# Performance work log

Measured on AMD Instinct MI355X. Metric: run time of the kernel, lower is better.

Reference implementation:

```python
import jax, jax.numpy as jnp
import numpy as np

N_NODES = 100000
FEAT = 64
HID = 128
N_EDGES = 1200000


def setup_inputs() -> dict:
    key = jax.random.key(0)
    ks = jax.random.split(key, 8)
    x = jax.random.normal(ks[0], (N_NODES, FEAT), dtype=jnp.float32)
    edge_index = jax.random.randint(ks[1], (2, N_EDGES), 0, N_NODES, dtype=jnp.int32)
    # SAGEConv params: lin_l (on aggregated neighbors, with bias), lin_r (on root, no bias)
    W1l = jax.random.normal(ks[2], (HID, FEAT), jnp.float32) / np.float32(np.sqrt(FEAT))
    b1l = jnp.zeros((HID,), jnp.float32)
    W1r = jax.random.normal(ks[3], (HID, FEAT), jnp.float32) / np.float32(np.sqrt(FEAT))
    W2l = jax.random.normal(ks[4], (FEAT, HID), jnp.float32) / np.float32(np.sqrt(HID))
    b2l = jnp.zeros((FEAT,), jnp.float32)
    W2r = jax.random.normal(ks[5], (FEAT, HID), jnp.float32) / np.float32(np.sqrt(HID))
    return {"x": x, "edge_index": edge_index, "W1l": W1l, "b1l": b1l,
            "W1r": W1r, "W2l": W2l, "b2l": b2l, "W2r": W2r}


def _sage_conv(x, src, dst, Wl, bl, Wr, n_nodes):
    # mean aggregation of neighbor messages x[src] at targets dst
    msg = x[src]                                                  # [E, d]
    agg = jax.ops.segment_sum(msg, dst, num_segments=n_nodes)     # [N, d]
    deg = jax.ops.segment_sum(jnp.ones((src.shape[0],), x.dtype), dst,
                              num_segments=n_nodes)               # [N]
    agg = agg / jnp.maximum(deg, 1.0)[:, None]
    # out = lin_l(agg) + lin_r(x); lin_r has no bias (PyG SAGEConv default)
    return agg @ Wl.T + bl + x @ Wr.T


def reference(x, edge_index, W1l, b1l, W1r, W2l, b2l, W2r):
    src, dst = edge_index[0], edge_index[1]
    n = x.shape[0]
    h = jax.nn.relu(_sage_conv(x, src, dst, W1l, b1l, W1r, n))
    # dropout(p=0.5) is identity in eval mode
    out = _sage_conv(h, src, dst, W2l, b2l, W2r, n)
    return out
```

## Files before the change

### kernel.cpp

```cpp
#include <hip/hip_runtime.h>
#include <hip/hip_bf16.h>

typedef __bf16 bf16;
typedef __attribute__((ext_vector_type(8))) __bf16 bf16x8;
typedef __attribute__((ext_vector_type(4))) float f32x4;

#define NBLK 256

__device__ inline void unpack8(uint4 r, f32x4& a, f32x4& b) {
  a.x = __uint_as_float(r.x << 16);
  a.y = __uint_as_float(r.x & 0xffff0000u);
  a.z = __uint_as_float(r.y << 16);
  a.w = __uint_as_float(r.y & 0xffff0000u);
  b.x = __uint_as_float(r.z << 16);
  b.y = __uint_as_float(r.z & 0xffff0000u);
  b.z = __uint_as_float(r.w << 16);
  b.w = __uint_as_float(r.w & 0xffff0000u);
}

__device__ inline uint4 slot_load(const bf16* __restrict__ tab, const int* __restrict__ nbr,
                                  int base, int e, int q, int fo) {
  int idx = base + q;
  uint4 r = make_uint4(0u, 0u, 0u, 0u);
  if (idx < e) {
    int j = nbr[idx];
    r = *(const uint4*)(tab + j * 64 + fo);
  }
  return r;
}

__global__ __launch_bounds__(256) void setup_k(const float* __restrict__ x,
                                               const int* __restrict__ dst,
                                               const float* __restrict__ W1l,
                                               const float* __restrict__ W1r,
                                               const float* __restrict__ W2l,
                                               const float* __restrict__ W2r,
                                               bf16* __restrict__ xb,
                                               bf16* __restrict__ B1,
                                               bf16* __restrict__ B2,
                                               int* __restrict__ hist,
                                               int E, int nb, int N, int Np) {
  __shared__ int h[1024];
  int t = threadIdx.x;
  if (blockIdx.x < NBLK) {
    for (int i = t; i < nb; i += 256) h[i] = 0;
    __syncthreads();
    int chunk = (E + NBLK - 1) / NBLK;
    int s = blockIdx.x * chunk, e = min(E, s + chunk);
    for (int i = s + t; i < e; i += 256) atomicAdd(&h[dst[i] >> 7], 1);
    __syncthreads();
    for (int i = t; i < nb; i += 256) hist[(long)i * NBLK + blockIdx.x] = h[i];
  } else if (blockIdx.x < NBLK + 128) {
    int gid = (blockIdx.x - NBLK) * 256 + t;
    if (gid < 16384) {
      int c = gid >> 7, k = gid & 127;
      float v = (k < 64) ? W1l[c * 64 + k] : W1r[c * 64 + (k - 64)];
      B1[gid] = (bf16)v;
    } else {
      int idx = gid - 16384;
      int n = idx >> 7, k = idx & 127;
      float v = (n < 64) ? W2l[n * 128 + k] : W2r[(n - 64) * 128 + k];
      B2[idx] = (bf16)v;
    }
  } else {
    int gid = (blockIdx.x - NBLK - 128) * 256 + t;
    long base = (long)gid * 4;
    if (base >= (long)Np * 64) return;
    if (base < (long)N * 64) {
      f32x4 v = *(const f32x4*)(x + base);
      bf16 o[4] = {(bf16)v.x, (bf16)v.y, (bf16)v.z, (bf16)v.w};
      *(ulong1*)(xb + base) = *(ulong1*)o;
    } else {
      bf16 o[4] = {(bf16)0.0f, (bf16)0.0f, (bf16)0.0f, (bf16)0.0f};
      *(ulong1*)(xb + base) = *(ulong1*)o;
    }
  }
}

__global__ __launch_bounds__(256) void scanA_k(int* __restrict__ hist,
                                               int* __restrict__ bsum) {
  __shared__ int sd[256];
  int t = threadIdx.x;
  int idx = blockIdx.x * 256 + t;
  int v = hist[idx];
  sd[t] = v;
  __syncthreads();
#pragma unroll
  for (int off = 1; off < 256; off <<= 1) {
    int tv = (t >= off) ? sd[t - off] : 0;
    __syncthreads();
    if (t >= off) sd[t] += tv;
    __syncthreads();
  }
  hist[idx] = sd[t] - v;
  if (t == 255) bsum[blockIdx.x] = sd[255];
}

__global__ __launch_bounds__(1024) void scanB_k(int* __restrict__ bsum, int nb) {
  __shared__ int sd[1024];
  int t = threadIdx.x;
  int v = (t < nb) ? bsum[t] : 0;
  sd[t] = v;
  __syncthreads();
#pragma unroll
  for (int off = 1; off < 1024; off <<= 1) {
    int tv = (t >= off) ? sd[t - off] : 0;
    __syncthreads();
    if (t >= off) sd[t] += tv;
    __syncthreads();
  }
  if (t < nb) bsum[t] = sd[t] - v;
}

__global__ __launch_bounds__(512) void scat_k(const int* __restrict__ src,
                                              const int* __restrict__ dst,
                                              const int* __restrict__ hist,
                                              const int* __restrict__ bsum,
                                              unsigned* __restrict__ ebuf, int E, int nb) {
  __shared__ int cur[1024];
  for (int i = threadIdx.x; i < nb; i += 512)
    cur[i] = bsum[i] + hist[(long)i * NBLK + blockIdx.x];
  __syncthreads();
  int chunk = (E + NBLK - 1) / NBLK;
  int s = blockIdx.x * chunk, e = min(E, s + chunk);
  for (int i = s + threadIdx.x; i < e; i += 512) {
    int d = dst[i];
    int pos = atomicAdd(&cur[d >> 7], 1);
    ebuf[pos] = ((unsigned)src[i] << 7) | (unsigned)(d & 127);
  }
}

__global__ __launch_bounds__(256) void csr_k(const unsigned* __restrict__ ebuf,
                                             const int* __restrict__ bsum,
                                             int* __restrict__ rowptr,
                                             int* __restrict__ nbr, int nb, int Np, int E) {
  __shared__ int hcnt[128];
  __shared__ int hoff[128];
  int b = blockIdx.x, t = threadIdx.x;
  int s = bsum[b];
  int e = (b + 1 < nb) ? bsum[b + 1] : E;
  if (t < 128) hcnt[t] = 0;
  __syncthreads();
  for (int i = s + t; i < e; i += 256) atomicAdd(&hcnt[ebuf[i] & 127u], 1);
  __syncthreads();
  if (t < 128) hoff[t] = hcnt[t];
  __syncthreads();
#pragma unroll
  for (int off = 1; off < 128; off <<= 1) {
    int v = (t < 128 && t >= off) ? hoff[t - off] : 0;
    __syncthreads();
    if (t < 128 && t >= off) hoff[t] += v;
    __syncthreads();
  }
  if (t < 128) {
    int ex = hoff[t] - hcnt[t];
    rowptr[b * 128 + t] = s + ex;
    hcnt[t] = ex;
  }
  if (blockIdx.x == gridDim.x - 1 && t == 0) rowptr[Np] = E;
  __syncthreads();
  for (int i = s + t; i < e; i += 256) {
    unsigned r = ebuf[i];
    int pos = atomicAdd(&hcnt[r & 127u], 1);
    nbr[s + pos] = (int)(r >> 7);
  }
}

__global__ __launch_bounds__(256) void agg1_k(const bf16* __restrict__ xb,
                                              const int* __restrict__ rowptr,
                                              const int* __restrict__ nbr,
                                              bf16* __restrict__ A1, int Np) {
  int wave = threadIdx.x >> 6, lane = threadIdx.x & 63;
  int n = blockIdx.x * 4 + wave;
  if (n >= Np) return;
  int s = rowptr[n], e = rowptr[n + 1];
  int q = lane >> 3, f = lane & 7;
  int fo = f * 8;
  f32x4 sa = {0, 0, 0, 0}, sb = {0, 0, 0, 0};
  uint4 c0 = slot_load(xb, nbr, s, e, q, fo);
  uint4 c1 = slot_load(xb, nbr, s + 8, e, q, fo);
  int i = s + 16;
  for (; i < e; i += 16) {
    uint4 n0 = slot_load(xb, nbr, i, e, q, fo);
    uint4 n1 = slot_load(xb, nbr, i + 8, e, q, fo);
    f32x4 a, b;
    unpack8(c0, a, b); sa += a; sb += b;
    unpack8(c1, a, b); sa += a; sb += b;
    c0 = n0; c1 = n1;
  }
  {
    f32x4 a, b;
    unpack8(c0, a, b); sa += a; sb += b;
    unpack8(c1, a, b); sa += a; sb += b;
  }
  float v[8] = {sa.x, sa.y, sa.z, sa.w, sb.x, sb.y, sb.z, sb.w};
#pragma unroll
  for (int k = 0; k < 8; k++) {
    v[k] += __shfl_xor(v[k], 8);
    v[k] += __shfl_xor(v[k], 16);
    v[k] += __shfl_xor(v[k], 32);
  }
  float invd = 1.0f / fmaxf((float)(e - s), 1.0f);
  if (q == 0) {
    bf16x8 o = {(bf16)(v[0] * invd), (bf16)(v[1] * invd), (bf16)(v[2] * invd),
                (bf16)(v[3] * invd), (bf16)(v[4] * invd), (bf16)(v[5] * invd),
                (bf16)(v[6] * invd), (bf16)(v[7] * invd)};
    *(bf16x8*)(A1 + n * 128 + fo) = o;
  } else if (q == 1) {
    uint4 rv = *(const uint4*)(xb + n * 64 + fo);
    *(uint4*)(A1 + n * 128 + 64 + fo) = rv;
  }
}

__device__ inline int swzoff(int r, int x) {
  return r * 256 + (x ^ (((r & 3) << 6) ^ ((r & 7) << 4)));
}

__global__ __launch_bounds__(256) void fused_k(const bf16* __restrict__ A,
                                               const bf16* __restrict__ B1g,
                                               const bf16* __restrict__ B2g,
                                               const float* __restrict__ b1l,
                                               bf16* __restrict__ Ct,
                                               bf16* __restrict__ Cu, int T) {
  __shared__ __align__(16) char Asm[2][8192];
  __shared__ __align__(16) char Hsm[8192];
  int tid = threadIdx.x;
  int wave = tid >> 6, lane = tid & 63;
  int row = lane & 15, quad = lane >> 4;
  int cb = wave * 32;

  bf16x8 b1f[2][4], b2f[2][4];
#pragma unroll
  for (int jj = 0; jj < 2; jj++)
#pragma unroll
    for (int s = 0; s < 4; s++) {
      b1f[jj][s] = *(const bf16x8*)(B1g + (cb + jj * 16 + row) * 128 + s * 32 + quad * 8);
      b2f[jj][s] = *(const bf16x8*)(B2g + (cb + jj * 16 + row) * 128 + s * 32 + quad * 8);
    }
  float bias[2] = {b1l[cb + row], b1l[cb + 16 + row]};

  int srow = wave * 8 + quad;
  int schunk = row;

  int t = blockIdx.x;
  {
    uint4 v0 = *(const uint4*)(A + ((long)t * 32 + srow) * 128 + schunk * 8);
    uint4 v1 = *(const uint4*)(A + ((long)t * 32 + srow + 4) * 128 + schunk * 8);
    *(uint4*)(Asm[0] + swzoff(srow, schunk * 16)) = v0;
    *(uint4*)(Asm[0] + swzoff(srow + 4, schunk * 16)) = v1;
  }
  __syncthreads();

  int p = 0;
  for (; t < T; t += (int)gridDim.x, p ^= 1) {
    int tn = t + (int)gridDim.x;
    bool pf = tn < T;
    uint4 v0 = {}, v1 = {};
    if (pf) {
      v0 = *(const uint4*)(A + ((long)tn * 32 + srow) * 128 + schunk * 8);
      v1 = *(const uint4*)(A + ((long)tn * 32 + srow + 4) * 128 + schunk * 8);
    }
    f32x4 acc1[2][2] = {};
#pragma unroll
    for (int s = 0; s < 4; s++) {
#pragma unroll
      for (int st = 0; st < 2; st++) {
        bf16x8 a = *(const bf16x8*)(Asm[p] + swzoff(st * 16 + row, s * 64 + quad * 16));
#pragma unroll
        for (int jj = 0; jj < 2; jj++)
          acc1[st][jj] = __builtin_amdgcn_mfma_f32_16x16x32_bf16(a, b1f[jj][s], acc1[st][jj], 0, 0, 0);
      }
    }
#pragma unroll
    for (int st = 0; st < 2; st++)
#pragma unroll
      for (int jj = 0; jj < 2; jj++)
#pragma unroll
        for (int i = 0; i < 4; i++) {
          float v = acc1[st][jj][i] + bias[jj];
          v = v > 0.0f ? v : 0.0f;
          *(bf16*)(Hsm + swzoff(st * 16 + quad * 4 + i, (cb + jj * 16 + row) * 2)) = (bf16)v;
        }
    __syncthreads();
    f32x4 acc2[2][2] = {};
#pragma unroll
    for (int s = 0; s < 4; s++) {
#pragma unroll
      for (int st = 0; st < 2; st++) {
        bf16x8 a = *(const bf16x8*)(Hsm + swzoff(st * 16 + row, s * 64 + quad * 16));
#pragma unroll
        for (int jj = 0; jj < 2; jj++)
          acc2[st][jj] = __builtin_amdgcn_mfma_f32_16x16x32_bf16(a, b2f[jj][s], acc2[st][jj], 0, 0, 0);
      }
    }
    bf16* outp = (wave < 2) ? Ct : Cu;
    int oc = cb + row - ((wave < 2) ? 0 : 64);
#pragma unroll
    for (int st = 0; st < 2; st++)
#pragma unroll
      for (int jj = 0; jj < 2; jj++)
#pragma unroll
        for (int i = 0; i < 4; i++) {
          long grow = (long)t * 32 + st * 16 + quad * 4 + i;
          outp[grow * 64 + oc + jj * 16] = (bf16)acc2[st][jj][i];
        }
    if (pf) {
      *(uint4*)(Asm[p ^ 1] + swzoff(srow, schunk * 16)) = v0;
      *(uint4*)(Asm[p ^ 1] + swzoff(srow + 4, schunk * 16)) = v1;
    }
    __syncthreads();
  }
}

__global__ __launch_bounds__(256) void agg2_k(const bf16* __restrict__ tmat,
                                              const bf16* __restrict__ umat,
                                              const int* __restrict__ rowptr,
                                              const int* __restrict__ nbr,
                                              const float* __restrict__ b2l,
                                              float* __restrict__ out, int N) {
  int wave = threadIdx.x >> 6, lane = threadIdx.x & 63;
  int n = blockIdx.x * 4 + wave;
  if (n >= N) return;
  int s = rowptr[n], e = rowptr[n + 1];
  int q = lane >> 3, f = lane & 7;
  int fo = f * 8;
  f32x4 sa = {0, 0, 0, 0}, sb = {0, 0, 0, 0};
  uint4 c0 = slot_load(tmat, nbr, s, e, q, fo);
  uint4 c1 = slot_load(tmat, nbr, s + 8, e, q, fo);
  int i = s + 16;
  for (; i < e; i += 16) {
    uint4 n0 = slot_load(tmat, nbr, i, e, q, fo);
    uint4 n1 = slot_load(tmat, nbr, i + 8, e, q, fo);
    f32x4 a, b;
    unpack8(c0, a, b); sa += a; sb += b;
    unpack8(c1, a, b); sa += a; sb += b;
    c0 = n0; c1 = n1;
  }
  {
    f32x4 a, b;
    unpack8(c0, a, b); sa += a; sb += b;
    unpack8(c1, a, b); sa += a; sb += b;
  }
  float v[8] = {sa.x, sa.y, sa.z, sa.w, sb.x, sb.y, sb.z, sb.w};
#pragma unroll
  for (int k = 0; k < 8; k++) {
    v[k] += __shfl_xor(v[k], 8);
    v[k] += __shfl_xor(v[k], 16);
    v[k] += __shfl_xor(v[k], 32);
  }
  if (q == 0) {
    float invd = 1.0f / fmaxf((float)(e - s), 1.0f);
    f32x4 b0 = *(const f32x4*)(b2l + fo);
    f32x4 b1 = *(const f32x4*)(b2l + fo + 4);
    f32x4 ua, ub;
    unpack8(*(const uint4*)(umat + n * 64 + fo), ua, ub);
    f32x4 o0, o1;
    o0.x = v[0] * invd + b0.x + ua.x;
    o0.y = v[1] * invd + b0.y + ua.y;
    o0.z = v[2] * invd + b0.z + ua.z;
    o0.w = v[3] * invd + b0.w + ua.w;
    o1.x = v[4] * invd + b1.x + ub.x;
    o1.y = v[5] * invd + b1.y + ub.y;
    o1.z = v[6] * invd + b1.z + ub.z;
    o1.w = v[7] * invd + b1.w + ub.w;
    *(f32x4*)(out + n * 64 + fo) = o0;
    *(f32x4*)(out + n * 64 + fo + 4) = o1;
  }
}

static inline size_t align256(size_t x) { return (x + 255) / 256 * 256; }

extern "C" void kernel_launch(void* const* d_in, const int* in_sizes, int n_in,
                              void* d_out, int out_size, void* d_ws, size_t ws_size,
                              hipStream_t stream) {
  const float* x = (const float*)d_in[0];
  const int* edge_index = (const int*)d_in[1];
  const float* W1l = (const float*)d_in[2];
  const float* b1l = (const float*)d_in[3];
  const float* W1r = (const float*)d_in[4];
  const float* W2l = (const float*)d_in[5];
  const float* b2l = (const float*)d_in[6];
  const float* W2r = (const float*)d_in[7];

  const int N = in_sizes[0] / 64;
  const int E = in_sizes[1] / 2;
  const int Np = (N + 127) / 128 * 128;
  const int nb = Np / 128;
  const int M = nb * NBLK;

  const int* src = edge_index;
  const int* dst = edge_index + E;

  char* ws = (char*)d_ws;
  size_t off = 0;
  int* hist = (int*)(ws + off);           off += align256((size_t)M * 4);
  int* bsum = (int*)(ws + off);           off += align256((size_t)nb * 4);
  int* rowptr = (int*)(ws + off);         off += align256((size_t)(Np + 1) * 4);
  unsigned* ebuf = (unsigned*)(ws + off); off += align256((size_t)E * 4);
  int* nbr = (int*)(ws + off);            off += align256((size_t)E * 4);
  bf16* xb = (bf16*)(ws + off);           off += align256((size_t)Np * 64 * 2);
  bf16* A1 = (bf16*)(ws + off);           off += align256((size_t)Np * 128 * 2);
  bf16* tmat = (bf16*)(ws + off);         off += align256((size_t)Np * 64 * 2);
  bf16* umat = (bf16*)(ws + off);         off += align256((size_t)Np * 64 * 2);
  bf16* B1 = (bf16*)(ws + off);           off += align256(128 * 128 * 2);
  bf16* B2 = (bf16*)(ws + off);           off += align256(128 * 128 * 2);
  float* out = (float*)d_out;

  const int cvtBlocks = (int)(((long)Np * 64 / 4 + 255) / 256);
  setup_k<<<NBLK + 128 + cvtBlocks, 256, 0, stream>>>(x, dst, W1l, W1r, W2l, W2r,
                                                      xb, B1, B2, hist, E, nb, N, Np);
  scanA_k<<<nb, 256, 0, stream>>>(hist, bsum);
  scanB_k<<<1, 1024, 0, stream>>>(bsum, nb);
  scat_k<<<NBLK, 512, 0, stream>>>(src, dst, hist, bsum, ebuf, E, nb);
  csr_k<<<nb, 256, 0, stream>>>(ebuf, bsum, rowptr, nbr, nb, Np, E);

  agg1_k<<<Np / 4, 256, 0, stream>>>(xb, rowptr, nbr, A1, Np);
  fused_k<<<1024, 256, 0, stream>>>(A1, B1, B2, b1l, tmat, umat, Np / 32);
  agg2_k<<<(N + 3) / 4, 256, 0, stream>>>(tmat, umat, rowptr, nbr, b2l, out, N);
}
```

Measured before the change: 219.2 us.

## Process four nodes per wave in agg1 with cross-node software prefetch

Result: no change. 220.2 us (+0.4%).

```diff
diff --git a/kernel.cpp b/kernel.cpp
--- a/kernel.cpp
+++ b/kernel.cpp
@@ -171,44 +171,64 @@
                                               const int* __restrict__ nbr,
                                               bf16* __restrict__ A1, int Np) {
   int wave = threadIdx.x >> 6, lane = threadIdx.x & 63;
-  int n = blockIdx.x * 4 + wave;
-  if (n >= Np) return;
-  int s = rowptr[n], e = rowptr[n + 1];
+  int n0 = (blockIdx.x * 4 + wave) * 4;
+  if (n0 >= Np) return;
   int q = lane >> 3, f = lane & 7;
   int fo = f * 8;
-  f32x4 sa = {0, 0, 0, 0}, sb = {0, 0, 0, 0};
-  uint4 c0 = slot_load(xb, nbr, s, e, q, fo);
-  uint4 c1 = slot_load(xb, nbr, s + 8, e, q, fo);
-  int i = s + 16;
-  for (; i < e; i += 16) {
-    uint4 n0 = slot_load(xb, nbr, i, e, q, fo);
-    uint4 n1 = slot_load(xb, nbr, i + 8, e, q, fo);
-    f32x4 a, b;
-    unpack8(c0, a, b); sa += a; sb += b;
-    unpack8(c1, a, b); sa += a; sb += b;
-    c0 = n0; c1 = n1;
-  }
-  {
-    f32x4 a, b;
-    unpack8(c0, a, b); sa += a; sb += b;
-    unpack8(c1, a, b); sa += a; sb += b;
-  }
-  float v[8] = {sa.x, sa.y, sa.z, sa.w, sb.x, sb.y, sb.z, sb.w};
-#pragma unroll
-  for (int k = 0; k < 8; k++) {
-    v[k] += __shfl_xor(v[k], 8);
-    v[k] += __shfl_xor(v[k], 16);
-    v[k] += __shfl_xor(v[k], 32);
-  }
-  float invd = 1.0f / fmaxf((float)(e - s), 1.0f);
-  if (q == 0) {
-    bf16x8 o = {(bf16)(v[0] * invd), (bf16)(v[1] * invd), (bf16)(v[2] * invd),
-                (bf16)(v[3] * invd), (bf16)(v[4] * invd), (bf16)(v[5] * invd),
-                (bf16)(v[6] * invd), (bf16)(v[7] * invd)};
-    *(bf16x8*)(A1 + n * 128 + fo) = o;
-  } else if (q == 1) {
-    uint4 rv = *(const uint4*)(xb + n * 64 + fo);
-    *(uint4*)(A1 + n * 128 + 64 + fo) = rv;
+  int s[4], e[4];
+#pragma unroll
+  for (int m = 0; m < 4; m++) { s[m] = rowptr[n0 + m]; e[m] = rowptr[n0 + m + 1]; }
+  uint4 c0[4], c1[4];
+#pragma unroll
+  for (int m = 0; m < 2; m++) {
+    c0[m] = slot_load(xb, nbr, s[m], e[m], q, fo);
+    c1[m] = slot_load(xb, nbr, s[m] + 8, e[m], q, fo);
+  }
+  uint4 rvc = (q == 1) ? *(const uint4*)(xb + (long)n0 * 64 + fo)
+                       : make_uint4(0u, 0u, 0u, 0u);
+#pragma unroll
+  for (int m = 0; m < 4; m++) {
+    if (m + 2 < 4) {
+      c0[m + 2] = slot_load(xb, nbr, s[m + 2], e[m + 2], q, fo);
+      c1[m + 2] = slot_load(xb, nbr, s[m + 2] + 8, e[m + 2], q, fo);
+    }
+    uint4 rvn = (q == 1 && m + 1 < 4)
+                    ? *(const uint4*)(xb + (long)(n0 + m + 1) * 64 + fo)
+                    : make_uint4(0u, 0u, 0u, 0u);
+    f32x4 sa = {0, 0, 0, 0}, sb = {0, 0, 0, 0};
+    uint4 a0 = c0[m], a1 = c1[m];
+    if (s[m] + 16 < e[m]) {
+      for (int i = s[m] + 16; i < e[m]; i += 16) {
+        uint4 t0 = slot_load(xb, nbr, i, e[m], q, fo);
+        uint4 t1 = slot_load(xb, nbr, i + 8, e[m], q, fo);
+        f32x4 a, b;
+        unpack8(a0, a, b); sa += a; sb += b;
+        unpack8(a1, a, b); sa += a; sb += b;
+        a0 = t0; a1 = t1;
+      }
+    }
+    {
+      f32x4 a, b;
+      unpack8(a0, a, b); sa += a; sb += b;
+      unpack8(a1, a, b); sa += a; sb += b;
+    }
+    float v[8] = {sa.x, sa.y, sa.z, sa.w, sb.x, sb.y, sb.z, sb.w};
+#pragma unroll
+    for (int k = 0; k < 8; k++) {
+      v[k] += __shfl_xor(v[k], 8);
+      v[k] += __shfl_xor(v[k], 16);
+      v[k] += __shfl_xor(v[k], 32);
+    }
+    float invd = 1.0f / fmaxf((float)(e[m] - s[m]), 1.0f);
+    if (q == 0) {
+      bf16x8 o = {(bf16)(v[0] * invd), (bf16)(v[1] * invd), (bf16)(v[2] * invd),
+                  (bf16)(v[3] * invd), (bf16)(v[4] * invd), (bf16)(v[5] * invd),
+                  (bf16)(v[6] * invd), (bf16)(v[7] * invd)};
+      *(bf16x8*)(A1 + (long)(n0 + m) * 128 + fo) = o;
+    } else if (q == 1) {
+      *(uint4*)(A1 + (long)(n0 + m) * 128 + 64 + fo) = rvc;
+    }
+    rvc = rvn;
   }
 }
 
@@ -414,7 +434,7 @@
   scat_k<<<NBLK, 512, 0, stream>>>(src, dst, hist, bsum, ebuf, E, nb);
   csr_k<<<nb, 256, 0, stream>>>(ebuf, bsum, rowptr, nbr, nb, Np, E);
 
-  agg1_k<<<Np / 4, 256, 0, stream>>>(xb, rowptr, nbr, A1, Np);
-  fused_k<<<1024, 256, 0, stream>>>(A1, B1, B2, b1l, tmat, umat, Np / 32);
+  agg1_k<<<Np / 16, 256, 0, stream>>>(xb, rowptr, nbr, A1, Np);
+  fused_k<<<1564, 256, 0, stream>>>(A1, B1, B2, b1l, tmat, umat, Np / 32);
   agg2_k<<<(N + 3) / 4, 256, 0, stream>>>(tmat, umat, rowptr, nbr, b2l, out, N);
 }
```

## Fuse per-bucket CSR sort into both aggregation kernels via LDS neighbor lists

Applied to the files above, without the earlier changes.

Result: slower. 228.7 us (+4.3%).

```diff
diff --git a/kernel.cpp b/kernel.cpp
--- a/kernel.cpp
+++ b/kernel.cpp
@@ -6,6 +6,7 @@
 typedef __attribute__((ext_vector_type(4))) float f32x4;
 
 #define NBLK 256
+#define CAP 3072
 
 __device__ inline void unpack8(uint4 r, f32x4& a, f32x4& b) {
   a.x = __uint_as_float(r.x << 16);
@@ -18,13 +19,13 @@
   b.w = __uint_as_float(r.w & 0xffff0000u);
 }
 
-__device__ inline uint4 slot_load(const bf16* __restrict__ tab, const int* __restrict__ nbr,
-                                  int base, int e, int q, int fo) {
+__device__ inline uint4 lslot(const bf16* __restrict__ tab, const int* lnbr,
+                              int base, int e, int q, int fo) {
   int idx = base + q;
   uint4 r = make_uint4(0u, 0u, 0u, 0u);
   if (idx < e) {
-    int j = nbr[idx];
-    r = *(const uint4*)(tab + j * 64 + fo);
+    int j = lnbr[idx];
+    r = *(const uint4*)(tab + (long)j * 64 + fo);
   }
   return r;
 }
@@ -130,85 +131,92 @@
   }
 }
 
-__global__ __launch_bounds__(256) void csr_k(const unsigned* __restrict__ ebuf,
-                                             const int* __restrict__ bsum,
-                                             int* __restrict__ rowptr,
-                                             int* __restrict__ nbr, int nb, int Np, int E) {
+__device__ inline void bucket_sort(const unsigned* __restrict__ ebuf, int s, int e,
+                                   int t, int* hcnt, int* hoff, int* lnbr) {
+  if (t < 128) hcnt[t] = 0;
+  __syncthreads();
+  for (int i = s + t; i < e; i += 512) atomicAdd(&hcnt[ebuf[i] & 127u], 1);
+  __syncthreads();
+  if (t < 128) hoff[t + 1] = hcnt[t];
+  if (t == 0) hoff[0] = 0;
+  __syncthreads();
+#pragma unroll
+  for (int off = 1; off < 128; off <<= 1) {
+    int v = (t < 128 && t >= off) ? hoff[t + 1 - off] : 0;
+    __syncthreads();
+    if (t < 128 && t >= off) hoff[t + 1] += v;
+    __syncthreads();
+  }
+  if (t < 128) hcnt[t] = hoff[t];
+  __syncthreads();
+  for (int i = s + t; i < e; i += 512) {
+    unsigned r = ebuf[i];
+    int pos = atomicAdd(&hcnt[r & 127u], 1);
+    lnbr[pos] = (int)(r >> 7);
+  }
+  __syncthreads();
+}
+
+__global__ __launch_bounds__(512) void bagg1_k(const bf16* __restrict__ xb,
+                                               const unsigned* __restrict__ ebuf,
+                                               const int* __restrict__ bsum,
+                                               bf16* __restrict__ A1, int nb, int E) {
   __shared__ int hcnt[128];
-  __shared__ int hoff[128];
+  __shared__ int hoff[129];
+  __shared__ int lnbr[CAP];
   int b = blockIdx.x, t = threadIdx.x;
   int s = bsum[b];
   int e = (b + 1 < nb) ? bsum[b + 1] : E;
-  if (t < 128) hcnt[t] = 0;
-  __syncthreads();
-  for (int i = s + t; i < e; i += 256) atomicAdd(&hcnt[ebuf[i] & 127u], 1);
-  __syncthreads();
-  if (t < 128) hoff[t] = hcnt[t];
-  __syncthreads();
-#pragma unroll
-  for (int off = 1; off < 128; off <<= 1) {
-    int v = (t < 128 && t >= off) ? hoff[t - off] : 0;
-    __syncthreads();
-    if (t < 128 && t >= off) hoff[t] += v;
-    __syncthreads();
-  }
-  if (t < 128) {
-    int ex = hoff[t] - hcnt[t];
-    rowptr[b * 128 + t] = s + ex;
-    hcnt[t] = ex;
-  }
-  if (blockIdx.x == gridDim.x - 1 && t == 0) rowptr[Np] = E;
-  __syncthreads();
-  for (int i = s + t; i < e; i += 256) {
-    unsigned r = ebuf[i];
-    int pos = atomicAdd(&hcnt[r & 127u], 1);
-    nbr[s + pos] = (int)(r >> 7);
-  }
-}
-
-__global__ __launch_bounds__(256) void agg1_k(const bf16* __restrict__ xb,
-                                              const int* __restrict__ rowptr,
-                                              const int* __restrict__ nbr,
-                                              bf16* __restrict__ A1, int Np) {
-  int wave = threadIdx.x >> 6, lane = threadIdx.x & 63;
-  int n = blockIdx.x * 4 + wave;
-  if (n >= Np) return;
-  int s = rowptr[n], e = rowptr[n + 1];
-  int q = lane >> 3, f = lane & 7;
-  int fo = f * 8;
-  f32x4 sa = {0, 0, 0, 0}, sb = {0, 0, 0, 0};
-  uint4 c0 = slot_load(xb, nbr, s, e, q, fo);
-  uint4 c1 = slot_load(xb, nbr, s + 8, e, q, fo);
-  int i = s + 16;
-  for (; i < e; i += 16) {
-    uint4 n0 = slot_load(xb, nbr, i, e, q, fo);
-    uint4 n1 = slot_load(xb, nbr, i + 8, e, q, fo);
-    f32x4 a, b;
-    unpack8(c0, a, b); sa += a; sb += b;
-    unpack8(c1, a, b); sa += a; sb += b;
-    c0 = n0; c1 = n1;
-  }
-  {
-    f32x4 a, b;
-    unpack8(c0, a, b); sa += a; sb += b;
-    unpack8(c1, a, b); sa += a; sb += b;
-  }
-  float v[8] = {sa.x, sa.y, sa.z, sa.w, sb.x, sb.y, sb.z, sb.w};
-#pragma unroll
-  for (int k = 0; k < 8; k++) {
-    v[k] += __shfl_xor(v[k], 8);
-    v[k] += __shfl_xor(v[k], 16);
-    v[k] += __shfl_xor(v[k], 32);
-  }
-  float invd = 1.0f / fmaxf((float)(e - s), 1.0f);
-  if (q == 0) {
-    bf16x8 o = {(bf16)(v[0] * invd), (bf16)(v[1] * invd), (bf16)(v[2] * invd),
-                (bf16)(v[3] * invd), (bf16)(v[4] * invd), (bf16)(v[5] * invd),
-                (bf16)(v[6] * invd), (bf16)(v[7] * invd)};
-    *(bf16x8*)(A1 + n * 128 + fo) = o;
-  } else if (q == 1) {
-    uint4 rv = *(const uint4*)(xb + n * 64 + fo);
-    *(uint4*)(A1 + n * 128 + 64 + fo) = rv;
+  if (e - s > CAP) e = s + CAP;
+  bucket_sort(ebuf, s, e, t, hcnt, hoff, lnbr);
+
+  int wave = t >> 6, lane = t & 63;
+  int q = lane >> 3, f = lane & 7, fo = f * 8;
+  int ls = hoff[wave * 16], le = hoff[wave * 16 + 1];
+  uint4 c0 = lslot(xb, lnbr, ls, le, q, fo);
+  uint4 c1 = lslot(xb, lnbr, ls + 8, le, q, fo);
+  for (int mm = 0; mm < 16; mm++) {
+    int lsN = 0, leN = 0;
+    if (mm < 15) { lsN = hoff[wave * 16 + mm + 1]; leN = hoff[wave * 16 + mm + 2]; }
+    uint4 n0 = lslot(xb, lnbr, lsN, leN, q, fo);
+    uint4 n1 = lslot(xb, lnbr, lsN + 8, leN, q, fo);
+    f32x4 sa = {0, 0, 0, 0}, sb = {0, 0, 0, 0};
+    if (ls + 16 < le) {
+      uint4 a0 = c0, a1 = c1;
+      for (int i = ls + 16; i < le; i += 16) {
+        uint4 t0 = lslot(xb, lnbr, i, le, q, fo);
+        uint4 t1 = lslot(xb, lnbr, i + 8, le, q, fo);
+        f32x4 a, bb;
+        unpack8(a0, a, bb); sa += a; sb += bb;
+        unpack8(a1, a, bb); sa += a; sb += bb;
+        a0 = t0; a1 = t1;
+      }
+      c0 = a0; c1 = a1;
+    }
+    {
+      f32x4 a, bb;
+      unpack8(c0, a, bb); sa += a; sb += bb;
+      unpack8(c1, a, bb); sa += a; sb += bb;
+    }
+    float v[8] = {sa.x, sa.y, sa.z, sa.w, sb.x, sb.y, sb.z, sb.w};
+#pragma unroll
+    for (int k = 0; k < 8; k++) {
+      v[k] += __shfl_xor(v[k], 8);
+      v[k] += __shfl_xor(v[k], 16);
+      v[k] += __shfl_xor(v[k], 32);
+    }
+    long n = (long)b * 128 + wave * 16 + mm;
+    float invd = 1.0f / fmaxf((float)(le - ls), 1.0f);
+    if (q == 0) {
+      bf16x8 o = {(bf16)(v[0] * invd), (bf16)(v[1] * invd), (bf16)(v[2] * invd),
+                  (bf16)(v[3] * invd), (bf16)(v[4] * invd), (bf16)(v[5] * invd),
+                  (bf16)(v[6] * invd), (bf16)(v[7] * invd)};
+      *(bf16x8*)(A1 + n * 128 + fo) = o;
+    } else if (q == 1) {
+      uint4 rv = *(const uint4*)(xb + n * 64 + fo);
+      *(uint4*)(A1 + n * 128 + 64 + fo) = rv;
+    }
+    c0 = n0; c1 = n1; ls = lsN; le = leN;
   }
 }
 
@@ -312,59 +320,77 @@
   }
 }
 
-__global__ __launch_bounds__(256) void agg2_k(const bf16* __restrict__ tmat,
-                                              const bf16* __restrict__ umat,
-                                              const int* __restrict__ rowptr,
-                                              const int* __restrict__ nbr,
-                                              const float* __restrict__ b2l,
-                                              float* __restrict__ out, int N) {
-  int wave = threadIdx.x >> 6, lane = threadIdx.x & 63;
-  int n = blockIdx.x * 4 + wave;
-  if (n >= N) return;
-  int s = rowptr[n], e = rowptr[n + 1];
-  int q = lane >> 3, f = lane & 7;
-  int fo = f * 8;
-  f32x4 sa = {0, 0, 0, 0}, sb = {0, 0, 0, 0};
-  uint4 c0 = slot_load(tmat, nbr, s, e, q, fo);
-  uint4 c1 = slot_load(tmat, nbr, s + 8, e, q, fo);
-  int i = s + 16;
-  for (; i < e; i += 16) {
-    uint4 n0 = slot_load(tmat, nbr, i, e, q, fo);
-    uint4 n1 = slot_load(tmat, nbr, i + 8, e, q, fo);
-    f32x4 a, b;
-    unpack8(c0, a, b); sa += a; sb += b;
-    unpack8(c1, a, b); sa += a; sb += b;
-    c0 = n0; c1 = n1;
-  }
-  {
-    f32x4 a, b;
-    unpack8(c0, a, b); sa += a; sb += b;
-    unpack8(c1, a, b); sa += a; sb += b;
-  }
-  float v[8] = {sa.x, sa.y, sa.z, sa.w, sb.x, sb.y, sb.z, sb.w};
-#pragma unroll
-  for (int k = 0; k < 8; k++) {
-    v[k] += __shfl_xor(v[k], 8);
-    v[k] += __shfl_xor(v[k], 16);
-    v[k] += __shfl_xor(v[k], 32);
-  }
-  if (q == 0) {
-    float invd = 1.0f / fmaxf((float)(e - s), 1.0f);
-    f32x4 b0 = *(const f32x4*)(b2l + fo);
-    f32x4 b1 = *(const f32x4*)(b2l + fo + 4);
-    f32x4 ua, ub;
-    unpack8(*(const uint4*)(umat + n * 64 + fo), ua, ub);
-    f32x4 o0, o1;
-    o0.x = v[0] * invd + b0.x + ua.x;
-    o0.y = v[1] * invd + b0.y + ua.y;
-    o0.z = v[2] * invd + b0.z + ua.z;
-    o0.w = v[3] * invd + b0.w + ua.w;
-    o1.x = v[4] * invd + b1.x + ub.x;
-    o1.y = v[5] * invd + b1.y + ub.y;
-    o1.z = v[6] * invd + b1.z + ub.z;
-    o1.w = v[7] * invd + b1.w + ub.w;
-    *(f32x4*)(out + n * 64 + fo) = o0;
-    *(f32x4*)(out + n * 64 + fo + 4) = o1;
+__global__ __launch_bounds__(512) void bagg2_k(const bf16* __restrict__ tmat,
+                                               const bf16* __restrict__ umat,
+                                               const unsigned* __restrict__ ebuf,
+                                               const int* __restrict__ bsum,
+                                               const float* __restrict__ b2l,
+                                               float* __restrict__ out,
+                                               int nb, int N, int E) {
+  __shared__ int hcnt[128];
+  __shared__ int hoff[129];
+  __shared__ int lnbr[CAP];
+  int b = blockIdx.x, t = threadIdx.x;
+  int s = bsum[b];
+  int e = (b + 1 < nb) ? bsum[b + 1] : E;
+  if (e - s > CAP) e = s + CAP;
+  bucket_sort(ebuf, s, e, t, hcnt, hoff, lnbr);
+
+  int wave = t >> 6, lane = t & 63;
+  int q = lane >> 3, f = lane & 7, fo = f * 8;
+  int ls = hoff[wave * 16], le = hoff[wave * 16 + 1];
+  uint4 c0 = lslot(tmat, lnbr, ls, le, q, fo);
+  uint4 c1 = lslot(tmat, lnbr, ls + 8, le, q, fo);
+  for (int mm = 0; mm < 16; mm++) {
+    int lsN = 0, leN = 0;
+    if (mm < 15) { lsN = hoff[wave * 16 + mm + 1]; leN = hoff[wave * 16 + mm + 2]; }
+    uint4 n0 = lslot(tmat, lnbr, lsN, leN, q, fo);
+    uint4 n1 = lslot(tmat, lnbr, lsN + 8, leN, q, fo);
+    f32x4 sa = {0, 0, 0, 0}, sb = {0, 0, 0, 0};
+    if (ls + 16 < le) {
+      uint4 a0 = c0, a1 = c1;
+      for (int i = ls + 16; i < le; i += 16) {
+        uint4 t0 = lslot(tmat, lnbr, i, le, q, fo);
+        uint4 t1 = lslot(tmat, lnbr, i + 8, le, q, fo);
+        f32x4 a, bb;
+        unpack8(a0, a, bb); sa += a; sb += bb;
+        unpack8(a1, a, bb); sa += a; sb += bb;
+        a0 = t0; a1 = t1;
+      }
+      c0 = a0; c1 = a1;
+    }
+    {
+      f32x4 a, bb;
+      unpack8(c0, a, bb); sa += a; sb += bb;
+      unpack8(c1, a, bb); sa += a; sb += bb;
+    }
+    float v[8] = {sa.x, sa.y, sa.z, sa.w, sb.x, sb.y, sb.z, sb.w};
+#pragma unroll
+    for (int k = 0; k < 8; k++) {
+      v[k] += __shfl_xor(v[k], 8);
+      v[k] += __shfl_xor(v[k], 16);
+      v[k] += __shfl_xor(v[k], 32);
+    }
+    long n = (long)b * 128 + wave * 16 + mm;
+    if (q == 0 && n < N) {
+      float invd = 1.0f / fmaxf((float)(le - ls), 1.0f);
+      f32x4 b0 = *(const f32x4*)(b2l + fo);
+      f32x4 b1 = *(const f32x4*)(b2l + fo + 4);
+      f32x4 ua, ub;
+      unpack8(*(const uint4*)(umat + n * 64 + fo), ua, ub);
+      f32x4 o0, o1;
+      o0.x = v[0] * invd + b0.x + ua.x;
+      o0.y = v[1] * invd + b0.y + ua.y;
+      o0.z = v[2] * invd + b0.z + ua.z;
+      o0.w = v[3] * invd + b0.w + ua.w;
+      o1.x = v[4] * invd + b1.x + ub.x;
+      o1.y = v[5] * invd + b1.y + ub.y;
+      o1.z = v[6] * invd + b1.z + ub.z;
+      o1.w = v[7] * invd + b1.w + ub.w;
+      *(f32x4*)(out + n * 64 + fo) = o0;
+      *(f32x4*)(out + n * 64 + fo + 4) = o1;
+    }
+    c0 = n0; c1 = n1; ls = lsN; le = leN;
   }
 }
 
@@ -395,9 +421,7 @@
   size_t off = 0;
   int* hist = (int*)(ws + off);           off += align256((size_t)M * 4);
   int* bsum = (int*)(ws + off);           off += align256((size_t)nb * 4);
-  int* rowptr = (int*)(ws + off);         off += align256((size_t)(Np + 1) * 4);
   unsigned* ebuf = (unsigned*)(ws + off); off += align256((size_t)E * 4);
-  int* nbr = (int*)(ws + off);            off += align256((size_t)E * 4);
   bf16* xb = (bf16*)(ws + off);           off += align256((size_t)Np * 64 * 2);
   bf16* A1 = (bf16*)(ws + off);           off += align256((size_t)Np * 128 * 2);
   bf16* tmat = (bf16*)(ws + off);         off += align256((size_t)Np * 64 * 2);
@@ -412,9 +436,8 @@
   scanA_k<<<nb, 256, 0, stream>>>(hist, bsum);
   scanB_k<<<1, 1024, 0, stream>>>(bsum, nb);
   scat_k<<<NBLK, 512, 0, stream>>>(src, dst, hist, bsum, ebuf, E, nb);
-  csr_k<<<nb, 256, 0, stream>>>(ebuf, bsum, rowptr, nbr, nb, Np, E);
-
-  agg1_k<<<Np / 4, 256, 0, stream>>>(xb, rowptr, nbr, A1, Np);
-  fused_k<<<1024, 256, 0, stream>>>(A1, B1, B2, b1l, tmat, umat, Np / 32);
-  agg2_k<<<(N + 3) / 4, 256, 0, stream>>>(tmat, umat, rowptr, nbr, b2l, out, N);
-}
+
+  bagg1_k<<<nb, 512, 0, stream>>>(xb, ebuf, bsum, A1, nb, E);
+  fused_k<<<1564, 256, 0, stream>>>(A1, B1, B2, b1l, tmat, umat, Np / 32);
+  bagg2_k<<<nb, 512, 0, stream>>>(tmat, umat, ebuf, bsum, b2l, out, nb, N, E);
+}
```
